# Performance work log

Measured on AMD Instinct MI355X. Metric: run time of the kernel, lower is better.

The kernel has to match this reference:

```python
import jax, jax.numpy as jnp
import numpy as np

N_PAIRS = 100000
N_TRIP = 500000
PAIR_DIM = 128
GEOM_DIM = 4


def _mlp(x, w1, b1, w2, b2):
    return jax.nn.silu(x @ w1 + b1) @ w2 + b2


def setup_inputs() -> dict:
    key = jax.random.key(0)
    ks = jax.random.split(key, 16)

    def lin(k, fan_in, fan_out):
        bound = 1.0 / np.sqrt(fan_in)
        kw, kb = jax.random.split(k)
        w = jax.random.uniform(kw, (fan_in, fan_out), jnp.float32, -bound, bound)
        b = jax.random.uniform(kb, (fan_out,), jnp.float32, -bound, bound)
        return w, b

    psi_w1, psi_b1 = lin(ks[0], 3 * PAIR_DIM + GEOM_DIM, PAIR_DIM)
    psi_w2, psi_b2 = lin(ks[1], PAIR_DIM, PAIR_DIM)
    phi_w1, phi_b1 = lin(ks[2], 2 * PAIR_DIM, PAIR_DIM)
    phi_w2, phi_b2 = lin(ks[3], PAIR_DIM, PAIR_DIM)

    return {
        "h_pair": jax.random.normal(ks[4], (N_PAIRS, PAIR_DIM), jnp.float32),
        "pair_vu_idx": jax.random.randint(ks[5], (N_TRIP,), 0, N_PAIRS, jnp.int64 if jax.config.jax_enable_x64 else jnp.int32).astype(jnp.int32),
        "pair_uw_idx": jax.random.randint(ks[6], (N_TRIP,), 0, N_PAIRS).astype(jnp.int32),
        "pair_vw_idx": jax.random.randint(ks[7], (N_TRIP,), 0, N_PAIRS).astype(jnp.int32),
        "geom_features": jax.random.normal(ks[8], (N_TRIP, GEOM_DIM), jnp.float32),
        "psi_w1": psi_w1, "psi_b1": psi_b1, "psi_w2": psi_w2, "psi_b2": psi_b2,
        "phi_w1": phi_w1, "phi_b1": phi_b1, "phi_w2": phi_w2, "phi_b2": phi_b2,
    }


def reference(h_pair, pair_vu_idx, pair_uw_idx, pair_vw_idx, geom_features,
              psi_w1, psi_b1, psi_w2, psi_b2,
              phi_w1, phi_b1, phi_w2, phi_b2):
    # gather triplet endpoints: [T, pair_dim] each
    h_vu = h_pair[pair_vu_idx]
    h_uw = h_pair[pair_uw_idx]
    h_vw = h_pair[pair_vw_idx]
    triplet_input = jnp.concatenate([h_vu, h_uw, h_vw, geom_features], axis=-1)  # [T, 3D+G]
    m_triplet = _mlp(triplet_input, psi_w1, psi_b1, psi_w2, psi_b2)  # [T, D]
    # scatter-add back onto pairs indexed by vw
    agg = jax.ops.segment_sum(m_triplet, pair_vw_idx, num_segments=h_pair.shape[0])  # [N, D]
    updated = _mlp(jnp.concatenate([h_pair, agg], axis=-1), phi_w1, phi_b1, phi_w2, phi_b2)
    return h_pair + updated
```

## Files before the change

kernel.cpp:

```cpp
#include <hip/hip_runtime.h>
#include <hip/hip_bf16.h>

#define T_TRIP 500000
#define NP     100000
#define NTILES 7813
#define NPAD   500032

typedef float f32x4 __attribute__((ext_vector_type(4)));
typedef __bf16 bf16x8 __attribute__((ext_vector_type(8)));
typedef unsigned short u16;
typedef unsigned short u16x8 __attribute__((ext_vector_type(8)));
typedef unsigned int u32;

__device__ __forceinline__ u16 f2bf(float f) {
  union { float f; unsigned u; } v; v.f = f;
  unsigned r = v.u + 0x7fffu + ((v.u >> 16) & 1u);
  return (u16)(r >> 16);
}

__device__ __forceinline__ ushort4 cvt4(float4 v) {
  ushort4 o; o.x = f2bf(v.x); o.y = f2bf(v.y); o.z = f2bf(v.z); o.w = f2bf(v.w);
  return o;
}

__device__ __forceinline__ u16 cvt1_pk(float v) {
  unsigned r;
  asm("v_cvt_pk_bf16_f32 %0, %1, %1" : "=v"(r) : "v"(v));
  return (u16)r;
}

__device__ __forceinline__ float bflo(u32 d) {
  union { u32 u; float f; } v; v.u = d << 16; return v.f;
}
__device__ __forceinline__ float bfhi(u32 d) {
  union { u32 u; float f; } v; v.u = d & 0xffff0000u; return v.f;
}

#define MFMA16(a, b, c) __builtin_amdgcn_mfma_f32_16x16x32_bf16((a), (b), (c), 0, 0, 0)

#define WAITVM(N) asm volatile("s_waitcnt vmcnt(" #N ")" ::: "memory")
#define LGKM0()   asm volatile("s_waitcnt lgkmcnt(0)" ::: "memory")

__device__ __forceinline__ void barrier_raw() {
  asm volatile("" ::: "memory");
  __builtin_amdgcn_s_barrier();
  asm volatile("" ::: "memory");
  __builtin_amdgcn_sched_barrier(0);
}

__device__ __forceinline__ void gload_lds16(const u16* g, u16* l) {
  __builtin_amdgcn_global_load_lds((const __attribute__((address_space(1))) void*)g,
                                   (__attribute__((address_space(3))) void*)l, 16, 0, 0);
}
__device__ __forceinline__ void gload_lds4(const int* g, int* l) {
  __builtin_amdgcn_global_load_lds((const __attribute__((address_space(1))) void*)g,
                                   (__attribute__((address_space(3))) void*)l, 4, 0, 0);
}

#define FP_W1A   0u
#define FP_W1B   16384u
#define FP_W1C   32768u
#define FP_W2    49152u
#define FP_PW1   65536u
#define FP_PW2   98304u
#define FP_W1D   114688u
#define FP_H     131072u
#define FP_AGG   12931072u
#define SB_CNT2    51462144ull
#define SB_CURSOR2 51862144ull
#define SB_BSUM2   52262144ull
#define SB_TRIP    52262656ull
#define WS_S2      60263168ull

#define HSTR   136
#define HSTR2  132
#define GSTR   520
#define X2STR  264

__global__ void k_pre(const float* __restrict__ psi_w1, const float* __restrict__ psi_w2,
                      const float* __restrict__ phi_w1, const float* __restrict__ phi_w2,
                      const float* __restrict__ h, const int* __restrict__ ivw,
                      u16* __restrict__ ws, int* __restrict__ cnt) {
  const int b = blockIdx.x;
  if (b < 450) {
    int i = b * 256 + threadIdx.x;
    if (i < 49152) {
      int s = i / 16384, r = i % 16384;
      int n = r / 128, k = r % 128;
      ws[FP_W1A + i] = f2bf(psi_w1[(s * 128 + k) * 128 + n]);
      return;
    }
    i -= 49152;
    if (i < 16384) {
      int n = i / 128, k = i % 128;
      ws[FP_W2 + i] = f2bf(psi_w2[k * 128 + n]);
      return;
    }
    i -= 16384;
    if (i < 32768) {
      int n = i / 256, k = i % 256;
      ws[FP_PW1 + i] = f2bf(phi_w1[k * 128 + n]);
      return;
    }
    i -= 32768;
    if (i < 16384) {
      int n = i / 128, k = i % 128;
      ws[FP_PW2 + i] = f2bf(phi_w2[k * 128 + n]);
      return;
    }
    i -= 16384;
    if (i < 512) {
      int k = i / 128, n = i % 128;
      reinterpret_cast<float*>(ws + FP_W1D)[i] = psi_w1[(384 + k) * 128 + n];
    }
  } else if (b < 6700) {
    const size_t i = (size_t)((b - 450) * 256 + threadIdx.x) * 8;
    float4 v0 = *reinterpret_cast<const float4*>(h + i);
    float4 v1 = *reinterpret_cast<const float4*>(h + i + 4);
    *reinterpret_cast<ushort4*>(ws + FP_H + i)     = cvt4(v0);
    *reinterpret_cast<ushort4*>(ws + FP_H + i + 4) = cvt4(v1);
    ushort4 z = {0, 0, 0, 0};
    *reinterpret_cast<ushort4*>(ws + FP_AGG + i)     = z;
    *reinterpret_cast<ushort4*>(ws + FP_AGG + i + 4) = z;
  } else {
    int i = (b - 6700) * 256 + threadIdx.x;
    if (i < T_TRIP) atomicAdd(&cnt[ivw[i]], 1);
  }
}

__global__ __launch_bounds__(1024) void k_scan1(const int* __restrict__ cnt,
                                                int* __restrict__ cursor, int* __restrict__ bsum) {
  __shared__ int wsum[16];
  const int idx = blockIdx.x * 1024 + threadIdx.x;
  const int lane = threadIdx.x & 63, wid = threadIdx.x >> 6;
  int v = (idx < NP) ? cnt[idx] : 0;
  int x = v;
#pragma unroll
  for (int off = 1; off < 64; off <<= 1) {
    int n = __shfl_up(x, off);
    if (lane >= off) x += n;
  }
  if (lane == 63) wsum[wid] = x;
  __syncthreads();
  if (threadIdx.x < 16) {
    int s = wsum[threadIdx.x];
#pragma unroll
    for (int off = 1; off < 16; off <<= 1) {
      int n = __shfl_up(s, off);
      if (threadIdx.x >= off) s += n;
    }
    wsum[threadIdx.x] = s;
  }
  __syncthreads();
  const int base = wid ? wsum[wid - 1] : 0;
  if (idx < NP) cursor[idx] = base + x - v;
  if (threadIdx.x == 1023) bsum[blockIdx.x] = base + x;
}

__global__ void k_scan2(int* __restrict__ bsum) {
  __shared__ int s[128];
  const int t = threadIdx.x;
  int v = (t < 98) ? bsum[t] : 0;
  s[t] = v; __syncthreads();
#pragma unroll
  for (int off = 1; off < 128; off <<= 1) {
    int a = (t >= off) ? s[t - off] : 0;
    __syncthreads();
    s[t] += a;
    __syncthreads();
  }
  if (t < 98) bsum[t] = s[t] - v;
}

__global__ void k_perm_pack(const int* __restrict__ ivu, const int* __restrict__ iuw,
                            const int* __restrict__ ivw, const float* __restrict__ geom,
                            int* __restrict__ cursor, const int* __restrict__ bsum,
                            int4* __restrict__ trip) {
  int i = blockIdx.x * 256 + threadIdx.x;
  if (i < T_TRIP) {
    int v = ivw[i];
    int pos = atomicAdd(&cursor[v], 1) + bsum[v >> 10];
    float4 g = reinterpret_cast<const float4*>(geom)[i];
    u32 pk0, pk1;
    asm("v_cvt_pk_bf16_f32 %0, %1, %2" : "=v"(pk0) : "v"(g.x), "v"(g.y));
    asm("v_cvt_pk_bf16_f32 %0, %1, %2" : "=v"(pk1) : "v"(g.z), "v"(g.w));
    int4 rec;
    rec.x = ivu[i] | ((v & 0x7fff) << 17);
    rec.y = iuw[i] | ((v >> 15) << 17);
    rec.z = (int)pk0;
    rec.w = (int)pk1;
    trip[pos] = rec;
  } else if (i < NPAD) {
    int4 z = {0, 0, 0, 0};
    trip[i] = z;
  }
}

__global__ __launch_bounds__(256, 2) void k_triplet_sortagg(
    const u16* __restrict__ H, const int* __restrict__ trip,
    const u16* __restrict__ W1A, const u16* __restrict__ W1B, const u16* __restrict__ W1C,
    const float* __restrict__ w1dF, const u16* __restrict__ W2T,
    const float* __restrict__ b1, const float* __restrict__ b2,
    u16* __restrict__ AGG) {
  __shared__ __align__(16) u16 XB[3][16 * GSTR];
  __shared__ __align__(16) u16 hl[64 * HSTR2];
  __shared__ __align__(16) int aosT[2][256];

  u32* mlu = reinterpret_cast<u32*>(hl);

  const int tid = threadIdx.x;
  const int w = tid >> 6, l = tid & 63;
  const int lr = l & 15;
  const int lk = (l >> 4) << 3;
  const int n0 = w * 32 + lr;
  const int rowh = (l >> 4) << 2;
  const int srow = l >> 4;
  const int schunk = (l & 15) ^ ((l >> 4) << 1);

  bf16x8 w2f[4][2];
#pragma unroll
  for (int ks = 0; ks < 4; ++ks)
#pragma unroll
    for (int ct = 0; ct < 2; ++ct)
      w2f[ks][ct] = *reinterpret_cast<const bf16x8*>(&W2T[(size_t)(n0 + ct * 16) * 128 + ks * 32 + lk]);
  const float b1v[2] = {b1[n0], b1[n0 + 16]};
  const float b2v[2] = {b2[n0], b2[n0 + 16]};
  float w1dv[4][2];
#pragma unroll
  for (int k = 0; k < 4; ++k) {
    w1dv[k][0] = w1dF[k * 128 + n0];
    w1dv[k][1] = w1dF[k * 128 + n0 + 16];
  }

  auto get_idx = [&](int cb, int r, int sel) -> int {
    if (sel == 0) return aosT[cb][r * 4] & 0x1FFFF;
    if (sel == 1) return aosT[cb][r * 4 + 1] & 0x1FFFF;
    u32 d0 = (u32)aosT[cb][r * 4], d1 = (u32)aosT[cb][r * 4 + 1];
    return (int)((d0 >> 17) | ((d1 >> 17) << 15));
  };

  auto stage_src = [&](int cb, int sel, int buf) {
#pragma unroll
    for (int q = 0; q < 4; ++q) {
      const int g = w * 4 + q;
      const int idx = get_idx(cb, g * 4 + srow, sel);
      gload_lds16(H + (size_t)idx * 128 + schunk * 8, &XB[buf][g * GSTR]);
    }
  };

  auto stage_aos = [&](int tile, int cb) {
    const int* src = trip + (size_t)tile * 256;
    gload_lds4(src + w * 64 + l, &aosT[cb][w * 64]);
  };

  auto gemm_src = [&](const u16* WT, int buf, f32x4 (&acc)[4][2]) {
#pragma unroll
    for (int ks = 0; ks < 4; ++ks) {
      bf16x8 a[4], b[2];
#pragma unroll
      for (int rt = 0; rt < 4; ++rt) {
        const int r = rt * 16 + lr;
        const int g = r >> 2, s = r & 3;
        const int j = ks * 4 + (l >> 4);
        a[rt] = *reinterpret_cast<const bf16x8*>(&XB[buf][g * GSTR + s * 128 + ((j ^ (s << 1)) << 3)]);
      }
#pragma unroll
      for (int ct = 0; ct < 2; ++ct)
        b[ct] = *reinterpret_cast<const bf16x8*>(&WT[(size_t)(n0 + ct * 16) * 128 + ks * 32 + lk]);
#pragma unroll
      for (int rt = 0; rt < 4; ++rt)
#pragma unroll
        for (int ct = 0; ct < 2; ++ct)
          acc[rt][ct] = MFMA16(a[rt], b[ct], acc[rt][ct]);
    }
  };

  int cur = 0;
  int tt = blockIdx.x;
  const int G = gridDim.x;

  {
    int t1 = tt + G; if (t1 >= NTILES) t1 = NTILES - 1;
    stage_aos(tt, 0);
    stage_aos(t1, 1);
    WAITVM(0);
    barrier_raw();
  }

  for (; tt < NTILES; tt += G) {
    const int t0 = tt * 64;

    stage_src(cur, 0, 0);
    stage_src(cur, 1, 1);
    stage_src(cur, 2, 2);
    WAITVM(0);
    barrier_raw();

    f32x4 acc[4][2] = {};
    gemm_src(W1A, 0, acc);
    gemm_src(W1B, 1, acc);
    gemm_src(W1C, 2, acc);

#pragma unroll
    for (int rt = 0; rt < 4; ++rt)
#pragma unroll
      for (int j = 0; j < 4; ++j) {
        const int row = rt * 16 + rowh + j;
        const u32 d2 = (u32)aosT[cur][row * 4 + 2];
        const u32 d3 = (u32)aosT[cur][row * 4 + 3];
        const float gx = bflo(d2), gy = bfhi(d2), gz = bflo(d3), gw = bfhi(d3);
#pragma unroll
        for (int ct = 0; ct < 2; ++ct)
          acc[rt][ct][j] += gx * w1dv[0][ct] + gy * w1dv[1][ct] +
                            gz * w1dv[2][ct] + gw * w1dv[3][ct];
      }
#pragma unroll
    for (int rt = 0; rt < 4; ++rt)
#pragma unroll
      for (int ct = 0; ct < 2; ++ct) {
        const float bb = b1v[ct];
#pragma unroll
        for (int j = 0; j < 4; ++j) {
          float v = acc[rt][ct][j] + bb;
          v = v * __builtin_amdgcn_rcpf(1.f + __expf(-v));
          hl[(rt * 16 + rowh + j) * HSTR2 + n0 + ct * 16] = cvt1_pk(v);
        }
      }
    LGKM0();
    barrier_raw();

    f32x4 acc2[4][2] = {};
#pragma unroll
    for (int ks = 0; ks < 4; ++ks) {
      bf16x8 a[4];
#pragma unroll
      for (int rt = 0; rt < 4; ++rt)
        a[rt] = *reinterpret_cast<const bf16x8*>(&hl[(rt * 16 + lr) * HSTR2 + ks * 32 + lk]);
#pragma unroll
      for (int rt = 0; rt < 4; ++rt)
#pragma unroll
        for (int ct = 0; ct < 2; ++ct)
          acc2[rt][ct] = MFMA16(a[rt], w2f[ks][ct], acc2[rt][ct]);
    }
    barrier_raw();

#pragma unroll
    for (int rt = 0; rt < 4; ++rt)
#pragma unroll
      for (int j = 0; j < 4; ++j) {
        const int row = rt * 16 + rowh + j;
        float v0 = acc2[rt][0][j] + b2v[0];
        float v1 = acc2[rt][1][j] + b2v[1];
        float x0 = __shfl_xor(v0, 1);
        float x1 = __shfl_xor(v1, 1);
        const bool even = (l & 1) == 0;
        float lo = even ? v0 : x1;
        float hi = even ? x0 : v1;
        const int dcol = even ? (n0 >> 1) : ((n0 + 15) >> 1);
        u32 pk;
        asm("v_cvt_pk_bf16_f32 %0, %1, %2" : "=v"(pk) : "v"(lo), "v"(hi));
        mlu[row * 66 + dcol] = pk;
      }
    LGKM0();
    barrier_raw();

    {
      u32 md[16];
#pragma unroll
      for (int r8 = 0; r8 < 16; ++r8)
        md[r8] = mlu[(w * 16 + r8) * 66 + l];
      int vws[16];
#pragma unroll
      for (int r8 = 0; r8 < 16; ++r8) {
        const int r = w * 16 + r8;
        const u32 d0 = (u32)aosT[cur][r * 4], d1 = (u32)aosT[cur][r * 4 + 1];
        vws[r8] = (int)((d0 >> 17) | ((d1 >> 17) << 15));
      }
      float lo = 0.f, hi = 0.f;
#pragma unroll
      for (int r8 = 0; r8 < 16; ++r8) {
        const int row = w * 16 + r8;
        if (t0 + row < T_TRIP) { lo += bflo(md[r8]); hi += bfhi(md[r8]); }
        const bool flush = (r8 == 15) || (vws[(r8 + 1) & 15] != vws[r8] || r8 == 15);
        if ((r8 == 15) || (vws[r8 + 1 > 15 ? 15 : r8 + 1] != vws[r8]) || flush == false) {
        }
        bool doflush;
        if (r8 == 15) doflush = true;
        else doflush = (vws[r8 + 1] != vws[r8]);
        if (doflush) {
          u16* p = AGG + (size_t)vws[r8] * 128 + l * 2;
          u32 pk;
          asm("v_cvt_pk_bf16_f32 %0, %1, %2" : "=v"(pk) : "v"(lo), "v"(hi));
          asm volatile("global_atomic_pk_add_bf16 %0, %1, off" :: "v"(p), "v"(pk) : "memory");
          lo = 0.f; hi = 0.f;
        }
      }
    }
    barrier_raw();

    {
      int t2 = tt + 2 * G; if (t2 >= NTILES) t2 = NTILES - 1;
      stage_aos(t2, cur);
    }

    WAITVM(0);
    barrier_raw();
    cur ^= 1;
  }
  WAITVM(0);
}

__global__ __launch_bounds__(256, 3) void k_pair_fast(
    const float* __restrict__ h_pair, const u16* __restrict__ H, const u16* __restrict__ AGG,
    const u16* __restrict__ PW1T, const u16* __restrict__ PW2T,
    const float* __restrict__ b1, const float* __restrict__ b2,
    float* __restrict__ out) {
  __shared__ __align__(16) u16 xl[64 * X2STR];
  __shared__ __align__(16) u16 hl[64 * HSTR];

  const int tid = threadIdx.x;
  const int r0 = blockIdx.x * 64;

  {
    const int row = tid >> 2, q = tid & 3;
    int rc = r0 + row; rc = (rc < NP) ? rc : (NP - 1);
    const u16x8* sh = reinterpret_cast<const u16x8*>(H + (size_t)rc * 128 + q * 32);
    const u16x8* sa = reinterpret_cast<const u16x8*>(AGG + (size_t)rc * 128 + q * 32);
    u16x8* d1 = reinterpret_cast<u16x8*>(&xl[row * X2STR + q * 32]);
    u16x8* d2 = reinterpret_cast<u16x8*>(&xl[row * X2STR + 128 + q * 32]);
#pragma unroll
    for (int i = 0; i < 4; ++i) { d1[i] = sh[i]; d2[i] = sa[i]; }
  }
  __syncthreads();

  const int w = tid >> 6, l = tid & 63;
  const int lr = l & 15;
  const int lk = (l >> 4) << 3;
  const int n0 = w * 32 + lr;
  const int rowh = (l >> 4) << 2;

  f32x4 acc[4][2] = {};
#pragma unroll 1
  for (int ks = 0; ks < 8; ++ks) {
    const int k0 = ks * 32;
    bf16x8 a[4], b[2];
#pragma unroll
    for (int rt = 0; rt < 4; ++rt)
      a[rt] = *reinterpret_cast<const bf16x8*>(&xl[(rt * 16 + lr) * X2STR + k0 + lk]);
#pragma unroll
    for (int ct = 0; ct < 2; ++ct)
      b[ct] = *reinterpret_cast<const bf16x8*>(&PW1T[(size_t)(n0 + ct * 16) * 256 + k0 + lk]);
#pragma unroll
    for (int rt = 0; rt < 4; ++rt)
#pragma unroll
      for (int ct = 0; ct < 2; ++ct)
        acc[rt][ct] = MFMA16(a[rt], b[ct], acc[rt][ct]);
  }

  {
    const float b1v0 = b1[n0], b1v1 = b1[n0 + 16];
#pragma unroll
    for (int rt = 0; rt < 4; ++rt)
#pragma unroll
      for (int ct = 0; ct < 2; ++ct) {
        const float bb = ct ? b1v1 : b1v0;
#pragma unroll
        for (int j = 0; j < 4; ++j) {
          float v = acc[rt][ct][j] + bb;
          v = v * __builtin_amdgcn_rcpf(1.f + __expf(-v));
          hl[(rt * 16 + rowh + j) * HSTR + n0 + ct * 16] = cvt1_pk(v);
        }
      }
  }
  __syncthreads();

  f32x4 acc2[4][2] = {};
#pragma unroll
  for (int ks = 0; ks < 4; ++ks) {
    const int k0 = ks * 32;
    bf16x8 a[4], b[2];
#pragma unroll
    for (int rt = 0; rt < 4; ++rt)
      a[rt] = *reinterpret_cast<const bf16x8*>(&hl[(rt * 16 + lr) * HSTR + k0 + lk]);
#pragma unroll
    for (int ct = 0; ct < 2; ++ct)
      b[ct] = *reinterpret_cast<const bf16x8*>(&PW2T[(size_t)(n0 + ct * 16) * 128 + k0 + lk]);
#pragma unroll
    for (int rt = 0; rt < 4; ++rt)
#pragma unroll
      for (int ct = 0; ct < 2; ++ct)
        acc2[rt][ct] = MFMA16(a[rt], b[ct], acc2[rt][ct]);
  }

  {
    const float b2v0 = b2[n0], b2v1 = b2[n0 + 16];
#pragma unroll
    for (int rt = 0; rt < 4; ++rt)
#pragma unroll
      for (int j = 0; j < 4; ++j) {
        const int row = rt * 16 + rowh + j;
        const int r = r0 + row;
        if (r < NP) {
          out[(size_t)r * 128 + n0]      = h_pair[(size_t)r * 128 + n0]      + acc2[rt][0][j] + b2v0;
          out[(size_t)r * 128 + n0 + 16] = h_pair[(size_t)r * 128 + n0 + 16] + acc2[rt][1][j] + b2v1;
        }
      }
  }
}

#define PSI_W1T_OFF 0
#define PSI_W2T_OFF 53248
#define PHI_W1T_OFF 69632
#define PHI_W2T_OFF 102400
#define WS_U16_TOTAL 118784
#define XSTR 424

__global__ void k_prep(const float* __restrict__ psi_w1, const float* __restrict__ psi_w2,
                       const float* __restrict__ phi_w1, const float* __restrict__ phi_w2,
                       u16* __restrict__ ws) {
  int i = blockIdx.x * 256 + threadIdx.x;
  if (i < 128 * 416) {
    int n = i / 416, k = i % 416;
    ws[PSI_W1T_OFF + i] = f2bf(k < 388 ? psi_w1[k * 128 + n] : 0.f);
    return;
  }
  i -= 128 * 416;
  if (i < 128 * 128) {
    int n = i / 128, k = i % 128;
    ws[PSI_W2T_OFF + i] = f2bf(psi_w2[k * 128 + n]);
    return;
  }
  i -= 128 * 128;
  if (i < 128 * 256) {
    int n = i / 256, k = i % 256;
    ws[PHI_W1T_OFF + i] = f2bf(phi_w1[k * 128 + n]);
    return;
  }
  i -= 128 * 256;
  if (i < 128 * 128) {
    int n = i / 128, k = i % 128;
    ws[PHI_W2T_OFF + i] = f2bf(phi_w2[k * 128 + n]);
  }
}

__global__ __launch_bounds__(256, 2) void k_triplet(
    const float* __restrict__ h_pair,
    const int* __restrict__ ivu, const int* __restrict__ iuw, const int* __restrict__ ivw,
    const float* __restrict__ geom,
    const u16* __restrict__ W1T, const u16* __restrict__ W2T,
    const float* __restrict__ b1, const float* __restrict__ b2,
    float* __restrict__ agg) {
  __shared__ __align__(16) u16 xl[64 * XSTR];
  __shared__ __align__(16) u16 hl[64 * HSTR];
  __shared__ int svw[64];

  const int tid = threadIdx.x;
  const int t0 = blockIdx.x * 64;

  {
    const int row = tid >> 2, q = tid & 3;
    const int t = t0 + row;
    const int tc = (t < T_TRIP) ? t : (T_TRIP - 1);
    if (q == 0) svw[row] = (t < T_TRIP) ? ivw[tc] : -1;
    int idx[3];
    idx[0] = ivu[tc]; idx[1] = iuw[tc]; idx[2] = ivw[tc];
#pragma unroll
    for (int s = 0; s < 3; ++s) {
      const float4* src = reinterpret_cast<const float4*>(h_pair + (size_t)idx[s] * 128 + q * 32);
      u16* dst = &xl[row * XSTR + s * 128 + q * 32];
#pragma unroll
      for (int i = 0; i < 8; ++i)
        *reinterpret_cast<ushort4*>(dst + i * 4) = cvt4(src[i]);
    }
  }
  if (tid < 64) {
    const int t = t0 + tid;
    const int tc = (t < T_TRIP) ? t : (T_TRIP - 1);
    const float4 g = reinterpret_cast<const float4*>(geom)[tc];
    u16* dst = &xl[tid * XSTR + 384];
    *reinterpret_cast<ushort4*>(dst) = cvt4(g);
    ushort4 z = {0, 0, 0, 0};
#pragma unroll
    for (int i = 1; i < 8; ++i) *reinterpret_cast<ushort4*>(dst + i * 4) = z;
  }
  __syncthreads();

  const int w = tid >> 6;
  const int l = tid & 63;
  const int lr = l & 15;
  const int lk = (l >> 4) << 3;
  const int n0 = w * 32 + lr;
  const int rowh = (l >> 4) << 2;

  f32x4 acc[4][2] = {};
#pragma unroll 1
  for (int ks = 0; ks < 13; ++ks) {
    const int k0 = ks * 32;
    bf16x8 a[4], b[2];
#pragma unroll
    for (int rt = 0; rt < 4; ++rt)
      a[rt] = *reinterpret_cast<const bf16x8*>(&xl[(rt * 16 + lr) * XSTR + k0 + lk]);
#pragma unroll
    for (int ct = 0; ct < 2; ++ct)
      b[ct] = *reinterpret_cast<const bf16x8*>(&W1T[(size_t)(n0 + ct * 16) * 416 + k0 + lk]);
#pragma unroll
    for (int rt = 0; rt < 4; ++rt)
#pragma unroll
      for (int ct = 0; ct < 2; ++ct)
        acc[rt][ct] = MFMA16(a[rt], b[ct], acc[rt][ct]);
  }

  {
    const float b1v0 = b1[n0], b1v1 = b1[n0 + 16];
#pragma unroll
    for (int rt = 0; rt < 4; ++rt)
#pragma unroll
      for (int ct = 0; ct < 2; ++ct) {
        const float bb = ct ? b1v1 : b1v0;
#pragma unroll
        for (int j = 0; j < 4; ++j) {
          float v = acc[rt][ct][j] + bb;
          v = v / (1.f + __expf(-v));
          hl[(rt * 16 + rowh + j) * HSTR + n0 + ct * 16] = f2bf(v);
        }
      }
  }
  __syncthreads();

  f32x4 acc2[4][2] = {};
#pragma unroll
  for (int ks = 0; ks < 4; ++ks) {
    const int k0 = ks * 32;
    bf16x8 a[4], b[2];
#pragma unroll
    for (int rt = 0; rt < 4; ++rt)
      a[rt] = *reinterpret_cast<const bf16x8*>(&hl[(rt * 16 + lr) * HSTR + k0 + lk]);
#pragma unroll
    for (int ct = 0; ct < 2; ++ct)
      b[ct] = *reinterpret_cast<const bf16x8*>(&W2T[(size_t)(n0 + ct * 16) * 128 + k0 + lk]);
#pragma unroll
    for (int rt = 0; rt < 4; ++rt)
#pragma unroll
      for (int ct = 0; ct < 2; ++ct)
        acc2[rt][ct] = MFMA16(a[rt], b[ct], acc2[rt][ct]);
  }

  {
    const float b2v0 = b2[n0], b2v1 = b2[n0 + 16];
#pragma unroll
    for (int rt = 0; rt < 4; ++rt)
#pragma unroll
      for (int j = 0; j < 4; ++j) {
        const int row = rt * 16 + rowh + j;
        const int dst = svw[row];
        if (dst >= 0) {
          unsafeAtomicAdd(&agg[(size_t)dst * 128 + n0], acc2[rt][0][j] + b2v0);
          unsafeAtomicAdd(&agg[(size_t)dst * 128 + n0 + 16], acc2[rt][1][j] + b2v1);
        }
      }
  }
}

__global__ __launch_bounds__(256, 2) void k_pair(
    const float* __restrict__ h_pair,
    const u16* __restrict__ W1T, const u16* __restrict__ W2T,
    const float* __restrict__ b1, const float* __restrict__ b2,
    float* __restrict__ out) {
  __shared__ __align__(16) u16 xl[64 * X2STR];
  __shared__ __align__(16) u16 hl[64 * HSTR];

  const int tid = threadIdx.x;
  const int r0 = blockIdx.x * 64;

  {
    const int row = tid >> 2, q = tid & 3;
    const int r = r0 + row;
    const int rc = (r < NP) ? r : (NP - 1);
    const float4* s1 = reinterpret_cast<const float4*>(h_pair + (size_t)rc * 128 + q * 32);
    const float4* s2 = reinterpret_cast<const float4*>(out + (size_t)rc * 128 + q * 32);
    u16* d1 = &xl[row * X2STR + q * 32];
    u16* d2 = &xl[row * X2STR + 128 + q * 32];
#pragma unroll
    for (int i = 0; i < 8; ++i) {
      *reinterpret_cast<ushort4*>(d1 + i * 4) = cvt4(s1[i]);
      *reinterpret_cast<ushort4*>(d2 + i * 4) = cvt4(s2[i]);
    }
  }
  __syncthreads();

  const int w = tid >> 6;
  const int l = tid & 63;
  const int lr = l & 15;
  const int lk = (l >> 4) << 3;
  const int n0 = w * 32 + lr;
  const int rowh = (l >> 4) << 2;

  f32x4 acc[4][2] = {};
#pragma unroll 1
  for (int ks = 0; ks < 8; ++ks) {
    const int k0 = ks * 32;
    bf16x8 a[4], b[2];
#pragma unroll
    for (int rt = 0; rt < 4; ++rt)
      a[rt] = *reinterpret_cast<const bf16x8*>(&xl[(rt * 16 + lr) * X2STR + k0 + lk]);
#pragma unroll
    for (int ct = 0; ct < 2; ++ct)
      b[ct] = *reinterpret_cast<const bf16x8*>(&W1T[(size_t)(n0 + ct * 16) * 256 + k0 + lk]);
#pragma unroll
    for (int rt = 0; rt < 4; ++rt)
#pragma unroll
      for (int ct = 0; ct < 2; ++ct)
        acc[rt][ct] = MFMA16(a[rt], b[ct], acc[rt][ct]);
  }

  {
    const float b1v0 = b1[n0], b1v1 = b1[n0 + 16];
#pragma unroll
    for (int rt = 0; rt < 4; ++rt)
#pragma unroll
      for (int ct = 0; ct < 2; ++ct) {
        const float bb = ct ? b1v1 : b1v0;
#pragma unroll
        for (int j = 0; j < 4; ++j) {
          float v = acc[rt][ct][j] + bb;
          v = v / (1.f + __expf(-v));
          hl[(rt * 16 + rowh + j) * HSTR + n0 + ct * 16] = f2bf(v);
        }
      }
  }
  __syncthreads();

  f32x4 acc2[4][2] = {};
#pragma unroll
  for (int ks = 0; ks < 4; ++ks) {
    const int k0 = ks * 32;
    bf16x8 a[4], b[2];
#pragma unroll
    for (int rt = 0; rt < 4; ++rt)
      a[rt] = *reinterpret_cast<const bf16x8*>(&hl[(rt * 16 + lr) * HSTR + k0 + lk]);
#pragma unroll
    for (int ct = 0; ct < 2; ++ct)
      b[ct] = *reinterpret_cast<const bf16x8*>(&W2T[(size_t)(n0 + ct * 16) * 128 + k0 + lk]);
#pragma unroll
    for (int rt = 0; rt < 4; ++rt)
#pragma unroll
      for (int ct = 0; ct < 2; ++ct)
        acc2[rt][ct] = MFMA16(a[rt], b[ct], acc2[rt][ct]);
  }

  {
    const float b2v0 = b2[n0], b2v1 = b2[n0 + 16];
#pragma unroll
    for (int rt = 0; rt < 4; ++rt)
#pragma unroll
      for (int j = 0; j < 4; ++j) {
        const int row = rt * 16 + rowh + j;
        const int r = r0 + row;
        if (r < NP) {
          out[(size_t)r * 128 + n0]      = h_pair[(size_t)r * 128 + n0]      + acc2[rt][0][j] + b2v0;
          out[(size_t)r * 128 + n0 + 16] = h_pair[(size_t)r * 128 + n0 + 16] + acc2[rt][1][j] + b2v1;
        }
      }
  }
}

extern "C" void kernel_launch(void* const* d_in, const int* in_sizes, int n_in,
                              void* d_out, int out_size, void* d_ws, size_t ws_size,
                              hipStream_t stream) {
  const float* h_pair = (const float*)d_in[0];
  const int* ivu = (const int*)d_in[1];
  const int* iuw = (const int*)d_in[2];
  const int* ivw = (const int*)d_in[3];
  const float* geom = (const float*)d_in[4];
  const float* psi_w1 = (const float*)d_in[5];
  const float* psi_b1 = (const float*)d_in[6];
  const float* psi_w2 = (const float*)d_in[7];
  const float* psi_b2 = (const float*)d_in[8];
  const float* phi_w1 = (const float*)d_in[9];
  const float* phi_b1 = (const float*)d_in[10];
  const float* phi_w2 = (const float*)d_in[11];
  const float* phi_b2 = (const float*)d_in[12];

  float* out = (float*)d_out;
  u16* ws = (u16*)d_ws;
  char* wsb = (char*)d_ws;

  if (ws_size >= WS_S2) {
    int*  cnt    = (int*)(wsb + SB_CNT2);
    int*  cursor = (int*)(wsb + SB_CURSOR2);
    int*  bsum   = (int*)(wsb + SB_BSUM2);
    int4* trip   = (int4*)(wsb + SB_TRIP);

    hipMemsetAsync(cnt, 0, NP * sizeof(int), stream);
    k_pre<<<8654, 256, 0, stream>>>(psi_w1, psi_w2, phi_w1, phi_w2, h_pair, ivw, ws, cnt);
    k_scan1<<<98, 1024, 0, stream>>>(cnt, cursor, bsum);
    k_scan2<<<1, 128, 0, stream>>>(bsum);
    k_perm_pack<<<(NPAD + 255) / 256, 256, 0, stream>>>(ivu, iuw, ivw, geom, cursor, bsum, trip);
    k_triplet_sortagg<<<512, 256, 0, stream>>>(
        ws + FP_H, (const int*)trip,
        ws + FP_W1A, ws + FP_W1B, ws + FP_W1C,
        reinterpret_cast<const float*>(ws + FP_W1D), ws + FP_W2,
        psi_b1, psi_b2, ws + FP_AGG);
    k_pair_fast<<<(NP + 63) / 64, 256, 0, stream>>>(
        h_pair, ws + FP_H, ws + FP_AGG,
        ws + FP_PW1, ws + FP_PW2, phi_b1, phi_b2, out);
  } else {
    hipMemsetAsync(d_out, 0, (size_t)out_size * sizeof(float), stream);
    k_prep<<<(WS_U16_TOTAL + 255) / 256, 256, 0, stream>>>(psi_w1, psi_w2, phi_w1, phi_w2, ws);
    k_triplet<<<(T_TRIP + 63) / 64, 256, 0, stream>>>(
        h_pair, ivu, iuw, ivw, geom,
        ws + PSI_W1T_OFF, ws + PSI_W2T_OFF, psi_b1, psi_b2, out);
    k_pair<<<(NP + 63) / 64, 256, 0, stream>>>(
        h_pair, ws + PHI_W1T_OFF, ws + PHI_W2T_OFF, phi_b1, phi_b2, out);
  }
}
```

Before: 295.4 us.

## Project pair features before gathering and apply second psi layer after aggregation

The first psi layer is split so that each pair row is multiplied by the three W1 blocks once, in a new k_proj kernel. A lightweight k_gsilu kernel then gathers the three projected rows per triplet, adds the geometry term and bias, applies SiLU, and scatter-adds the hidden activations. Because the second psi layer is linear, it moves into the pair kernel and runs on the aggregated sums, with psi_b2 scaled by each pair's triplet count. This cuts the dense matmul work from per-triplet to per-pair, at the cost of three extra bf16 intermediate buffers, a much larger workspace requirement, and extra bf16 rounding of the projections before they are summed.

```diff
diff --git a/kernel.cpp b/kernel.cpp
--- a/kernel.cpp
+++ b/kernel.cpp
@@ -5,6 +5,7 @@
 #define NP     100000
 #define NTILES 7813
 #define NPAD   500032
+#define NBATCH 31252
 
 typedef float f32x4 __attribute__((ext_vector_type(4)));
 typedef __bf16 bf16x8 __attribute__((ext_vector_type(8)));
@@ -37,25 +38,7 @@
 }
 
 #define MFMA16(a, b, c) __builtin_amdgcn_mfma_f32_16x16x32_bf16((a), (b), (c), 0, 0, 0)
-
-#define WAITVM(N) asm volatile("s_waitcnt vmcnt(" #N ")" ::: "memory")
 #define LGKM0()   asm volatile("s_waitcnt lgkmcnt(0)" ::: "memory")
-
-__device__ __forceinline__ void barrier_raw() {
-  asm volatile("" ::: "memory");
-  __builtin_amdgcn_s_barrier();
-  asm volatile("" ::: "memory");
-  __builtin_amdgcn_sched_barrier(0);
-}
-
-__device__ __forceinline__ void gload_lds16(const u16* g, u16* l) {
-  __builtin_amdgcn_global_load_lds((const __attribute__((address_space(1))) void*)g,
-                                   (__attribute__((address_space(3))) void*)l, 16, 0, 0);
-}
-__device__ __forceinline__ void gload_lds4(const int* g, int* l) {
-  __builtin_amdgcn_global_load_lds((const __attribute__((address_space(1))) void*)g,
-                                   (__attribute__((address_space(3))) void*)l, 4, 0, 0);
-}
 
 #define FP_W1A   0u
 #define FP_W1B   16384u
@@ -70,17 +53,18 @@
 #define SB_CURSOR2 51862144ull
 #define SB_BSUM2   52262144ull
 #define SB_TRIP    52262656ull
-#define WS_S2      60263168ull
+#define SB_YA      60263168ull
+#define SB_YB      85863168ull
+#define SB_YC     111463168ull
+#define WS_S3     137063168ull
 
 #define HSTR   136
-#define HSTR2  132
-#define GSTR   520
 #define X2STR  264
 
-__global__ void k_pre(const float* __restrict__ psi_w1, const float* __restrict__ psi_w2,
-                      const float* __restrict__ phi_w1, const float* __restrict__ phi_w2,
-                      const float* __restrict__ h, const int* __restrict__ ivw,
-                      u16* __restrict__ ws, int* __restrict__ cnt) {
+__global__ void k_pre3(const float* __restrict__ psi_w1, const float* __restrict__ psi_w2,
+                       const float* __restrict__ phi_w1, const float* __restrict__ phi_w2,
+                       const int* __restrict__ ivw,
+                       u16* __restrict__ ws, int* __restrict__ cnt) {
   const int b = blockIdx.x;
   if (b < 450) {
     int i = b * 256 + threadIdx.x;
@@ -113,17 +97,14 @@
       int k = i / 128, n = i % 128;
       reinterpret_cast<float*>(ws + FP_W1D)[i] = psi_w1[(384 + k) * 128 + n];
     }
-  } else if (b < 6700) {
-    const size_t i = (size_t)((b - 450) * 256 + threadIdx.x) * 8;
-    float4 v0 = *reinterpret_cast<const float4*>(h + i);
-    float4 v1 = *reinterpret_cast<const float4*>(h + i + 4);
-    *reinterpret_cast<ushort4*>(ws + FP_H + i)     = cvt4(v0);
-    *reinterpret_cast<ushort4*>(ws + FP_H + i + 4) = cvt4(v1);
+  } else if (b < 3575) {
+    const size_t i = (size_t)((b - 450) * 256 + threadIdx.x) * 16;
     ushort4 z = {0, 0, 0, 0};
-    *reinterpret_cast<ushort4*>(ws + FP_AGG + i)     = z;
-    *reinterpret_cast<ushort4*>(ws + FP_AGG + i + 4) = z;
+    u16* d = ws + FP_AGG + i;
+#pragma unroll
+    for (int k = 0; k < 4; ++k) *reinterpret_cast<ushort4*>(d + k * 4) = z;
   } else {
-    int i = (b - 6700) * 256 + threadIdx.x;
+    int i = (b - 3575) * 256 + threadIdx.x;
     if (i < T_TRIP) atomicAdd(&cnt[ivw[i]], 1);
   }
 }
@@ -196,248 +177,196 @@
   }
 }
 
-__global__ __launch_bounds__(256, 2) void k_triplet_sortagg(
-    const u16* __restrict__ H, const int* __restrict__ trip,
-    const u16* __restrict__ W1A, const u16* __restrict__ W1B, const u16* __restrict__ W1C,
-    const float* __restrict__ w1dF, const u16* __restrict__ W2T,
-    const float* __restrict__ b1, const float* __restrict__ b2,
-    u16* __restrict__ AGG) {
-  __shared__ __align__(16) u16 XB[3][16 * GSTR];
-  __shared__ __align__(16) u16 hl[64 * HSTR2];
-  __shared__ __align__(16) int aosT[2][256];
-
-  u32* mlu = reinterpret_cast<u32*>(hl);
-
+__global__ __launch_bounds__(256, 4) void k_proj(
+    const float* __restrict__ h, const u16* __restrict__ W1A, const u16* __restrict__ W1B,
+    const u16* __restrict__ W1C, u16* __restrict__ H,
+    u32* __restrict__ YA, u32* __restrict__ YB, u32* __restrict__ YC) {
+  __shared__ __align__(16) u16 xs[64 * 132];
   const int tid = threadIdx.x;
+  const int r0 = blockIdx.x * 64;
+  {
+    const int row = tid >> 2, q = tid & 3;
+    int rc = r0 + row; rc = (rc < NP) ? rc : (NP - 1);
+    const float4* src = reinterpret_cast<const float4*>(h + (size_t)rc * 128 + q * 32);
+    u16* ldst = &xs[row * 132 + q * 32];
+    u16* gdst = H + (size_t)rc * 128 + q * 32;
+#pragma unroll
+    for (int i = 0; i < 8; ++i) {
+      ushort4 c = cvt4(src[i]);
+      *reinterpret_cast<ushort4*>(ldst + i * 4) = c;
+      *reinterpret_cast<ushort4*>(gdst + i * 4) = c;
+    }
+  }
+  __syncthreads();
   const int w = tid >> 6, l = tid & 63;
-  const int lr = l & 15;
-  const int lk = (l >> 4) << 3;
+  const int lr = l & 15, lk = (l >> 4) << 3;
   const int n0 = w * 32 + lr;
   const int rowh = (l >> 4) << 2;
-  const int srow = l >> 4;
-  const int schunk = (l & 15) ^ ((l >> 4) << 1);
-
-  bf16x8 w2f[4][2];
-#pragma unroll
-  for (int ks = 0; ks < 4; ++ks)
-#pragma unroll
-    for (int ct = 0; ct < 2; ++ct)
-      w2f[ks][ct] = *reinterpret_cast<const bf16x8*>(&W2T[(size_t)(n0 + ct * 16) * 128 + ks * 32 + lk]);
-  const float b1v[2] = {b1[n0], b1[n0 + 16]};
-  const float b2v[2] = {b2[n0], b2[n0 + 16]};
-  float w1dv[4][2];
-#pragma unroll
-  for (int k = 0; k < 4; ++k) {
-    w1dv[k][0] = w1dF[k * 128 + n0];
-    w1dv[k][1] = w1dF[k * 128 + n0 + 16];
-  }
-
-  auto get_idx = [&](int cb, int r, int sel) -> int {
-    if (sel == 0) return aosT[cb][r * 4] & 0x1FFFF;
-    if (sel == 1) return aosT[cb][r * 4 + 1] & 0x1FFFF;
-    u32 d0 = (u32)aosT[cb][r * 4], d1 = (u32)aosT[cb][r * 4 + 1];
-    return (int)((d0 >> 17) | ((d1 >> 17) << 15));
-  };
-
-  auto stage_src = [&](int cb, int sel, int buf) {
-#pragma unroll
-    for (int q = 0; q < 4; ++q) {
-      const int g = w * 4 + q;
-      const int idx = get_idx(cb, g * 4 + srow, sel);
-      gload_lds16(H + (size_t)idx * 128 + schunk * 8, &XB[buf][g * GSTR]);
-    }
-  };
-
-  auto stage_aos = [&](int tile, int cb) {
-    const int* src = trip + (size_t)tile * 256;
-    gload_lds4(src + w * 64 + l, &aosT[cb][w * 64]);
-  };
-
-  auto gemm_src = [&](const u16* WT, int buf, f32x4 (&acc)[4][2]) {
+
+  const u16* WT[3] = {W1A, W1B, W1C};
+  u32* YT[3] = {YA, YB, YC};
+#pragma unroll
+  for (int s = 0; s < 3; ++s) {
+    f32x4 acc[4][2] = {};
 #pragma unroll
     for (int ks = 0; ks < 4; ++ks) {
       bf16x8 a[4], b[2];
 #pragma unroll
-      for (int rt = 0; rt < 4; ++rt) {
-        const int r = rt * 16 + lr;
-        const int g = r >> 2, s = r & 3;
-        const int j = ks * 4 + (l >> 4);
-        a[rt] = *reinterpret_cast<const bf16x8*>(&XB[buf][g * GSTR + s * 128 + ((j ^ (s << 1)) << 3)]);
-      }
+      for (int rt = 0; rt < 4; ++rt)
+        a[rt] = *reinterpret_cast<const bf16x8*>(&xs[(rt * 16 + lr) * 132 + ks * 32 + lk]);
 #pragma unroll
       for (int ct = 0; ct < 2; ++ct)
-        b[ct] = *reinterpret_cast<const bf16x8*>(&WT[(size_t)(n0 + ct * 16) * 128 + ks * 32 + lk]);
+        b[ct] = *reinterpret_cast<const bf16x8*>(&WT[s][(size_t)(n0 + ct * 16) * 128 + ks * 32 + lk]);
 #pragma unroll
       for (int rt = 0; rt < 4; ++rt)
 #pragma unroll
         for (int ct = 0; ct < 2; ++ct)
           acc[rt][ct] = MFMA16(a[rt], b[ct], acc[rt][ct]);
     }
-  };
-
-  int cur = 0;
-  int tt = blockIdx.x;
-  const int G = gridDim.x;
-
-  {
-    int t1 = tt + G; if (t1 >= NTILES) t1 = NTILES - 1;
-    stage_aos(tt, 0);
-    stage_aos(t1, 1);
-    WAITVM(0);
-    barrier_raw();
-  }
-
-  for (; tt < NTILES; tt += G) {
-    const int t0 = tt * 64;
-
-    stage_src(cur, 0, 0);
-    stage_src(cur, 1, 1);
-    stage_src(cur, 2, 2);
-    WAITVM(0);
-    barrier_raw();
-
-    f32x4 acc[4][2] = {};
-    gemm_src(W1A, 0, acc);
-    gemm_src(W1B, 1, acc);
-    gemm_src(W1C, 2, acc);
-
 #pragma unroll
     for (int rt = 0; rt < 4; ++rt)
 #pragma unroll
       for (int j = 0; j < 4; ++j) {
         const int row = rt * 16 + rowh + j;
-        const u32 d2 = (u32)aosT[cur][row * 4 + 2];
-        const u32 d3 = (u32)aosT[cur][row * 4 + 3];
-        const float gx = bflo(d2), gy = bfhi(d2), gz = bflo(d3), gw = bfhi(d3);
-#pragma unroll
-        for (int ct = 0; ct < 2; ++ct)
-          acc[rt][ct][j] += gx * w1dv[0][ct] + gy * w1dv[1][ct] +
-                            gz * w1dv[2][ct] + gw * w1dv[3][ct];
-      }
-#pragma unroll
-    for (int rt = 0; rt < 4; ++rt)
-#pragma unroll
-      for (int ct = 0; ct < 2; ++ct) {
-        const float bb = b1v[ct];
-#pragma unroll
-        for (int j = 0; j < 4; ++j) {
-          float v = acc[rt][ct][j] + bb;
-          v = v * __builtin_amdgcn_rcpf(1.f + __expf(-v));
-          hl[(rt * 16 + rowh + j) * HSTR2 + n0 + ct * 16] = cvt1_pk(v);
+        float v0 = acc[rt][0][j], v1 = acc[rt][1][j];
+        float x0 = __shfl_xor(v0, 1), x1 = __shfl_xor(v1, 1);
+        const bool even = (l & 1) == 0;
+        float lo = even ? v0 : x1, hi = even ? x0 : v1;
+        const int dcol = even ? (n0 >> 1) : ((n0 + 15) >> 1);
+        if (r0 + row < NP) {
+          u32 pk;
+          asm("v_cvt_pk_bf16_f32 %0, %1, %2" : "=v"(pk) : "v"(lo), "v"(hi));
+          YT[s][(size_t)(r0 + row) * 64 + dcol] = pk;
         }
       }
-    LGKM0();
-    barrier_raw();
-
-    f32x4 acc2[4][2] = {};
+  }
+}
+
+__global__ void k_gsilu(
+    const u32* __restrict__ YA, const u32* __restrict__ YB, const u32* __restrict__ YC,
+    const u32* __restrict__ tripw, const float* __restrict__ w1dF,
+    const float* __restrict__ b1, u16* __restrict__ Hagg) {
+  const int w = threadIdx.x >> 6, l = threadIdx.x & 63;
+  const int batch = blockIdx.x * 4 + w;
+  if (batch >= NBATCH) return;
+  const int t0 = batch * 16;
+
+  const u32 aos = tripw[(size_t)batch * 64 + l];
+
+  float wd[4][2];
+#pragma unroll
+  for (int k = 0; k < 4; ++k) {
+    wd[k][0] = w1dF[k * 128 + 2 * l];
+    wd[k][1] = w1dF[k * 128 + 2 * l + 1];
+  }
+  const float bb0 = b1[2 * l], bb1 = b1[2 * l + 1];
+
+  int vw[16];
+  u32 g2[16], g3[16], ga[16], gb[16], gc[16];
+#pragma unroll
+  for (int i = 0; i < 16; ++i) {
+    const u32 d0 = (u32)__shfl((int)aos, i * 4);
+    const u32 d1 = (u32)__shfl((int)aos, i * 4 + 1);
+    g2[i] = (u32)__shfl((int)aos, i * 4 + 2);
+    g3[i] = (u32)__shfl((int)aos, i * 4 + 3);
+    vw[i] = (int)((d0 >> 17) | ((d1 >> 17) << 15));
+    ga[i] = YA[(size_t)(d0 & 0x1FFFF) * 64 + l];
+    gb[i] = YB[(size_t)(d1 & 0x1FFFF) * 64 + l];
+    gc[i] = YC[(size_t)vw[i] * 64 + l];
+  }
+
+  float lo = 0.f, hi = 0.f;
+#pragma unroll
+  for (int i = 0; i < 16; ++i) {
+    if (t0 + i < T_TRIP) {
+      const float gx = bflo(g2[i]), gy = bfhi(g2[i]), gz = bflo(g3[i]), gw4 = bfhi(g3[i]);
+      float p0 = bflo(ga[i]) + bflo(gb[i]) + bflo(gc[i]) + bb0
+               + gx * wd[0][0] + gy * wd[1][0] + gz * wd[2][0] + gw4 * wd[3][0];
+      float p1 = bfhi(ga[i]) + bfhi(gb[i]) + bfhi(gc[i]) + bb1
+               + gx * wd[0][1] + gy * wd[1][1] + gz * wd[2][1] + gw4 * wd[3][1];
+      lo += p0 * __builtin_amdgcn_rcpf(1.f + __expf(-p0));
+      hi += p1 * __builtin_amdgcn_rcpf(1.f + __expf(-p1));
+    }
+    bool flush;
+    if (i == 15) flush = true; else flush = (vw[i + 1 < 16 ? i + 1 : 15] != vw[i]);
+    if (flush) {
+      u16* p = Hagg + (size_t)vw[i] * 128 + l * 2;
+      u32 pk;
+      asm("v_cvt_pk_bf16_f32 %0, %1, %2" : "=v"(pk) : "v"(lo), "v"(hi));
+      asm volatile("global_atomic_pk_add_bf16 %0, %1, off" :: "v"(p), "v"(pk) : "memory");
+      lo = 0.f; hi = 0.f;
+    }
+  }
+}
+
+__global__ __launch_bounds__(256, 3) void k_pair2(
+    const float* __restrict__ h_pair, const u16* __restrict__ H, const u16* __restrict__ Hagg,
+    const int* __restrict__ cnt, const u16* __restrict__ W2T,
+    const u16* __restrict__ PW1T, const u16* __restrict__ PW2T,
+    const float* __restrict__ psi_b2, const float* __restrict__ b1, const float* __restrict__ b2,
+    float* __restrict__ out) {
+  __shared__ __align__(16) u16 xl[64 * X2STR];
+  __shared__ __align__(16) u16 hl[64 * HSTR];
+  u32* xl32 = reinterpret_cast<u32*>(xl);
+
+  const int tid = threadIdx.x;
+  const int r0 = blockIdx.x * 64;
+
+  {
+    const int row = tid >> 2, q = tid & 3;
+    int rc = r0 + row; rc = (rc < NP) ? rc : (NP - 1);
+    const u16x8* sh = reinterpret_cast<const u16x8*>(H + (size_t)rc * 128 + q * 32);
+    const u16x8* sa = reinterpret_cast<const u16x8*>(Hagg + (size_t)rc * 128 + q * 32);
+    u16x8* d1 = reinterpret_cast<u16x8*>(&xl[row * X2STR + q * 32]);
+    u16x8* d2 = reinterpret_cast<u16x8*>(&hl[row * HSTR + q * 32]);
+#pragma unroll
+    for (int i = 0; i < 4; ++i) { d1[i] = sh[i]; d2[i] = sa[i]; }
+  }
+  __syncthreads();
+
+  const int w = tid >> 6, l = tid & 63;
+  const int lr = l & 15, lk = (l >> 4) << 3;
+  const int n0 = w * 32 + lr;
+  const int rowh = (l >> 4) << 2;
+
+  {
+    f32x4 acc[4][2] = {};
 #pragma unroll
     for (int ks = 0; ks < 4; ++ks) {
-      bf16x8 a[4];
+      bf16x8 a[4], b[2];
 #pragma unroll
       for (int rt = 0; rt < 4; ++rt)
-        a[rt] = *reinterpret_cast<const bf16x8*>(&hl[(rt * 16 + lr) * HSTR2 + ks * 32 + lk]);
+        a[rt] = *reinterpret_cast<const bf16x8*>(&hl[(rt * 16 + lr) * HSTR + ks * 32 + lk]);
+#pragma unroll
+      for (int ct = 0; ct < 2; ++ct)
+        b[ct] = *reinterpret_cast<const bf16x8*>(&W2T[(size_t)(n0 + ct * 16) * 128 + ks * 32 + lk]);
 #pragma unroll
       for (int rt = 0; rt < 4; ++rt)
 #pragma unroll
         for (int ct = 0; ct < 2; ++ct)
-          acc2[rt][ct] = MFMA16(a[rt], w2f[ks][ct], acc2[rt][ct]);
-    }
-    barrier_raw();
-
+          acc[rt][ct] = MFMA16(a[rt], b[ct], acc[rt][ct]);
+    }
+    const float pb2v[2] = {psi_b2[n0], psi_b2[n0 + 16]};
 #pragma unroll
     for (int rt = 0; rt < 4; ++rt)
 #pragma unroll
       for (int j = 0; j < 4; ++j) {
         const int row = rt * 16 + rowh + j;
-        float v0 = acc2[rt][0][j] + b2v[0];
-        float v1 = acc2[rt][1][j] + b2v[1];
-        float x0 = __shfl_xor(v0, 1);
-        float x1 = __shfl_xor(v1, 1);
+        int rc = r0 + row; rc = (rc < NP) ? rc : (NP - 1);
+        const float cf = (float)cnt[rc];
+        float v0 = acc[rt][0][j] + cf * pb2v[0];
+        float v1 = acc[rt][1][j] + cf * pb2v[1];
+        float x0 = __shfl_xor(v0, 1), x1 = __shfl_xor(v1, 1);
         const bool even = (l & 1) == 0;
-        float lo = even ? v0 : x1;
-        float hi = even ? x0 : v1;
+        float lo = even ? v0 : x1, hi = even ? x0 : v1;
         const int dcol = even ? (n0 >> 1) : ((n0 + 15) >> 1);
         u32 pk;
         asm("v_cvt_pk_bf16_f32 %0, %1, %2" : "=v"(pk) : "v"(lo), "v"(hi));
-        mlu[row * 66 + dcol] = pk;
+        xl32[row * (X2STR / 2) + 64 + dcol] = pk;
       }
-    LGKM0();
-    barrier_raw();
-
-    {
-      u32 md[16];
-#pragma unroll
-      for (int r8 = 0; r8 < 16; ++r8)
-        md[r8] = mlu[(w * 16 + r8) * 66 + l];
-      int vws[16];
-#pragma unroll
-      for (int r8 = 0; r8 < 16; ++r8) {
-        const int r = w * 16 + r8;
-        const u32 d0 = (u32)aosT[cur][r * 4], d1 = (u32)aosT[cur][r * 4 + 1];
-        vws[r8] = (int)((d0 >> 17) | ((d1 >> 17) << 15));
-      }
-      float lo = 0.f, hi = 0.f;
-#pragma unroll
-      for (int r8 = 0; r8 < 16; ++r8) {
-        const int row = w * 16 + r8;
-        if (t0 + row < T_TRIP) { lo += bflo(md[r8]); hi += bfhi(md[r8]); }
-        const bool flush = (r8 == 15) || (vws[(r8 + 1) & 15] != vws[r8] || r8 == 15);
-        if ((r8 == 15) || (vws[r8 + 1 > 15 ? 15 : r8 + 1] != vws[r8]) || flush == false) {
-        }
-        bool doflush;
-        if (r8 == 15) doflush = true;
-        else doflush = (vws[r8 + 1] != vws[r8]);
-        if (doflush) {
-          u16* p = AGG + (size_t)vws[r8] * 128 + l * 2;
-          u32 pk;
-          asm("v_cvt_pk_bf16_f32 %0, %1, %2" : "=v"(pk) : "v"(lo), "v"(hi));
-          asm volatile("global_atomic_pk_add_bf16 %0, %1, off" :: "v"(p), "v"(pk) : "memory");
-          lo = 0.f; hi = 0.f;
-        }
-      }
-    }
-    barrier_raw();
-
-    {
-      int t2 = tt + 2 * G; if (t2 >= NTILES) t2 = NTILES - 1;
-      stage_aos(t2, cur);
-    }
-
-    WAITVM(0);
-    barrier_raw();
-    cur ^= 1;
-  }
-  WAITVM(0);
-}
-
-__global__ __launch_bounds__(256, 3) void k_pair_fast(
-    const float* __restrict__ h_pair, const u16* __restrict__ H, const u16* __restrict__ AGG,
-    const u16* __restrict__ PW1T, const u16* __restrict__ PW2T,
-    const float* __restrict__ b1, const float* __restrict__ b2,
-    float* __restrict__ out) {
-  __shared__ __align__(16) u16 xl[64 * X2STR];
-  __shared__ __align__(16) u16 hl[64 * HSTR];
-
-  const int tid = threadIdx.x;
-  const int r0 = blockIdx.x * 64;
-
-  {
-    const int row = tid >> 2, q = tid & 3;
-    int rc = r0 + row; rc = (rc < NP) ? rc : (NP - 1);
-    const u16x8* sh = reinterpret_cast<const u16x8*>(H + (size_t)rc * 128 + q * 32);
-    const u16x8* sa = reinterpret_cast<const u16x8*>(AGG + (size_t)rc * 128 + q * 32);
-    u16x8* d1 = reinterpret_cast<u16x8*>(&xl[row * X2STR + q * 32]);
-    u16x8* d2 = reinterpret_cast<u16x8*>(&xl[row * X2STR + 128 + q * 32]);
-#pragma unroll
-    for (int i = 0; i < 4; ++i) { d1[i] = sh[i]; d2[i] = sa[i]; }
-  }
-  __syncthreads();
-
-  const int w = tid >> 6, l = tid & 63;
-  const int lr = l & 15;
-  const int lk = (l >> 4) << 3;
-  const int n0 = w * 32 + lr;
-  const int rowh = (l >> 4) << 2;
+  }
+  LGKM0();
+  __syncthreads();
 
   f32x4 acc[4][2] = {};
 #pragma unroll 1
@@ -785,25 +714,28 @@
   u16* ws = (u16*)d_ws;
   char* wsb = (char*)d_ws;
 
-  if (ws_size >= WS_S2) {
+  if (ws_size >= WS_S3) {
     int*  cnt    = (int*)(wsb + SB_CNT2);
     int*  cursor = (int*)(wsb + SB_CURSOR2);
     int*  bsum   = (int*)(wsb + SB_BSUM2);
     int4* trip   = (int4*)(wsb + SB_TRIP);
+    u32*  YA     = (u32*)(wsb + SB_YA);
+    u32*  YB     = (u32*)(wsb + SB_YB);
+    u32*  YC     = (u32*)(wsb + SB_YC);
 
     hipMemsetAsync(cnt, 0, NP * sizeof(int), stream);
-    k_pre<<<8654, 256, 0, stream>>>(psi_w1, psi_w2, phi_w1, phi_w2, h_pair, ivw, ws, cnt);
+    k_pre3<<<5529, 256, 0, stream>>>(psi_w1, psi_w2, phi_w1, phi_w2, ivw, ws, cnt);
     k_scan1<<<98, 1024, 0, stream>>>(cnt, cursor, bsum);
     k_scan2<<<1, 128, 0, stream>>>(bsum);
-    k_perm_pack<<<(NPAD + 255) / 256, 256, 0, stream>>>(ivu, iuw, ivw, geom, cursor, bsum, trip);
-    k_triplet_sortagg<<<512, 256, 0, stream>>>(
-        ws + FP_H, (const int*)trip,
-        ws + FP_W1A, ws + FP_W1B, ws + FP_W1C,
-        reinterpret_cast<const float*>(ws + FP_W1D), ws + FP_W2,
-        psi_b1, psi_b2, ws + FP_AGG);
-    k_pair_fast<<<(NP + 63) / 64, 256, 0, stream>>>(
-        h_pair, ws + FP_H, ws + FP_AGG,
-        ws + FP_PW1, ws + FP_PW2, phi_b1, phi_b2, out);
+    k_perm_pack<<<1954, 256, 0, stream>>>(ivu, iuw, ivw, geom, cursor, bsum, trip);
+    k_proj<<<1563, 256, 0, stream>>>(h_pair, ws + FP_W1A, ws + FP_W1B, ws + FP_W1C,
+                                     ws + FP_H, YA, YB, YC);
+    k_gsilu<<<(NBATCH + 3) / 4, 256, 0, stream>>>(
+        YA, YB, YC, (const u32*)trip,
+        reinterpret_cast<const float*>(ws + FP_W1D), psi_b1, ws + FP_AGG);
+    k_pair2<<<1563, 256, 0, stream>>>(
+        h_pair, ws + FP_H, ws + FP_AGG, cnt, ws + FP_W2,
+        ws + FP_PW1, ws + FP_PW2, psi_b2, phi_b1, phi_b2, out);
   } else {
     hipMemsetAsync(d_out, 0, (size_t)out_size * sizeof(float), stream);
     k_prep<<<(WS_U16_TOTAL + 255) / 256, 256, 0, stream>>>(psi_w1, psi_w2, phi_w1, phi_w2, ws);
```

New measurement: 288.0 us. 1.03x faster.
